# Performance work log

Measured on AMD Instinct MI355X. Metric: run time of the kernel, lower is better.

The kernel has to match this reference:

```python
import jax, jax.numpy as jnp
import numpy as np

INPUT_CHANNELS = 3

def setup_inputs() -> dict:
    key = jax.random.key(0)
    kx, ky = jax.random.split(key)
    x = jax.random.normal(kx, (8, 4096, 3), dtype=jnp.float32)
    y = jax.random.normal(ky, (8, 4096, 3), dtype=jnp.float32)
    return {"x": x, "y": y}

def reference(x, y):
    # Match torch: truncate both clouds to common num_points and input_channels.
    num_points = min(x.shape[1], y.shape[1])
    x = x[:, :num_points, :INPUT_CHANNELS]
    y = y[:, :num_points, :INPUT_CHANNELS]
    # pdist[b, i, j] = ||x_i||^2 + ||y_j||^2 - 2 x_i . y_j  (squared Euclidean)
    x2 = jnp.sum(x * x, axis=-1)          # [B, N]
    y2 = jnp.sum(y * y, axis=-1)          # [B, N]
    zz = jnp.einsum('bic,bjc->bij', x, y) # [B, N, N]
    pdist = x2[:, :, None] + y2[:, None, :] - 2.0 * zz
    # min over i (dim 1): nearest x for each y; min over j (dim 2): nearest y for each x
    loss = jnp.mean(jnp.min(pdist, axis=1)) + jnp.mean(jnp.min(pdist, axis=2))
    return loss * 0.005
```

## Files before the change

kernel.cpp:

```cpp
#include <hip/hip_runtime.h>

#define NPTS 4096
#define NB   8
#define TOT  (2 * NB * NPTS)

typedef __attribute__((ext_vector_type(8)))  short          bf16x8;
typedef __attribute__((ext_vector_type(8)))  unsigned short u16x8;
typedef __attribute__((ext_vector_type(16))) float          f32x16;

__device__ __forceinline__ unsigned short bf16_rne(float f) {
    unsigned u = __float_as_uint(f);
    u += 0x7FFFu + ((u >> 16) & 1u);
    return (unsigned short)(u >> 16);
}
__device__ __forceinline__ float bf16_f(unsigned short s) {
    return __uint_as_float(((unsigned)s) << 16);
}

__global__ __launch_bounds__(256) void prep_kernel(
    const float* __restrict__ x, const float* __restrict__ y,
    unsigned short* __restrict__ Aform, unsigned short* __restrict__ Bform,
    float* __restrict__ h32, unsigned* __restrict__ smax,
    float* __restrict__ out)
{
    int i   = blockIdx.x * 256 + threadIdx.x;
    int cid = i >> 12;
    int p   = i & 4095;
    const float* src = (cid < 8) ? x + ((size_t)cid * NPTS + p) * 3
                                 : y + ((size_t)(cid - 8) * NPTS + p) * 3;
    float c0 = src[0], c1 = src[1], c2 = src[2];
    float h  = -0.5f * (c0 * c0 + c1 * c1 + c2 * c2);

    unsigned short h0 = bf16_rne(c0), h1 = bf16_rne(c1), h2 = bf16_rne(c2);
    unsigned short l0 = bf16_rne(c0 - bf16_f(h0));
    unsigned short l1 = bf16_rne(c1 - bf16_f(h1));
    unsigned short l2 = bf16_rne(c2 - bf16_f(h2));
    unsigned short hh = bf16_rne(h);
    unsigned short hl = bf16_rne(h - bf16_f(hh));
    const unsigned short ONE = 0x3F80;

    u16x8 alo, ahi, blo, bhi;
    alo[0]=h0; alo[1]=h1; alo[2]=h2; alo[3]=l0; alo[4]=l1; alo[5]=l2; alo[6]=h0; alo[7]=h1;
    ahi[0]=h2; ahi[1]=ONE; ahi[2]=ONE; ahi[3]=0; ahi[4]=0; ahi[5]=0; ahi[6]=0; ahi[7]=0;
    blo[0]=h0; blo[1]=h1; blo[2]=h2; blo[3]=h0; blo[4]=h1; blo[5]=h2; blo[6]=l0; blo[7]=l1;
    bhi[0]=l2; bhi[1]=hh; bhi[2]=hl; bhi[3]=0; bhi[4]=0; bhi[5]=0; bhi[6]=0; bhi[7]=0;

    int u = p >> 5, pos = p & 31;
    size_t base = ((size_t)cid << 17) + (size_t)u * 1024 + (size_t)pos * 16;
    *(u16x8*)((char*)Aform + base)       = alo;
    *(u16x8*)((char*)Aform + base + 512) = ahi;
    *(u16x8*)((char*)Bform + base)       = blo;
    *(u16x8*)((char*)Bform + base + 512) = bhi;

    h32[i]  = h;
    smax[i] = 0u;
    if (i == 0) *out = 0.f;
}

__global__ __launch_bounds__(256, 2) void chamfer_mfma(
    const unsigned short* __restrict__ Aform,
    const unsigned short* __restrict__ Bform,
    unsigned* __restrict__ smax)
{
    __shared__ float buf[4][64][33];

    const int bid  = blockIdx.x;
    const int dirb = bid >> 6;
    const int sub  = bid & 63;
    const int iblk = sub >> 2;
    const int jq   = sub & 3;
    const int bcld = dirb ^ 8;

    const int tid = threadIdx.x;
    const int w   = tid >> 6;
    const int l   = tid & 63;
    const int g   = l >> 5;
    const int pos = l & 31;

    const char* Abase = (const char*)Aform + ((size_t)dirb << 17);
    const char* Bbase = (const char*)Bform + ((size_t)bcld << 17);

    const int it0 = iblk * 8 + w * 2;
    bf16x8 afr[2];
    #pragma unroll
    for (int t = 0; t < 2; ++t)
        afr[t] = *(const bf16x8*)(Abase + (size_t)(it0 + t) * 1024
                                        + (size_t)g * 512 + (size_t)pos * 16);

    f32x16 zc;
    #pragma unroll
    for (int r = 0; r < 16; ++r) zc[r] = 0.f;

    f32x16 run[2];
    #pragma unroll
    for (int t = 0; t < 2; ++t)
        #pragma unroll
        for (int r = 0; r < 16; ++r) run[t][r] = -3.0e38f;

    const char* Bq = Bbase + (size_t)(jq * 32) * 1024
                           + (size_t)g * 512 + (size_t)pos * 16;

    bf16x8 cb0 = *(const bf16x8*)(Bq);
    bf16x8 cb1 = *(const bf16x8*)(Bq + 1024);

    #pragma unroll 1
    for (int j = 0; j < 32; j += 2) {
        const int jn = (j + 2) & 31;
        bf16x8 nb0 = *(const bf16x8*)(Bq + (size_t)jn * 1024);
        bf16x8 nb1 = *(const bf16x8*)(Bq + (size_t)jn * 1024 + 1024);
        #pragma unroll
        for (int t = 0; t < 2; ++t) {
            f32x16 d0 = __builtin_amdgcn_mfma_f32_32x32x16_bf16(afr[t], cb0, zc, 0, 0, 0);
            f32x16 d1 = __builtin_amdgcn_mfma_f32_32x32x16_bf16(afr[t], cb1, zc, 0, 0, 0);
            #pragma unroll
            for (int r = 0; r < 16; ++r)
                run[t][r] = fmaxf(fmaxf(d0[r], d1[r]), run[t][r]);
        }
        cb0 = nb0; cb1 = nb1;
    }

    #pragma unroll
    for (int t = 0; t < 2; ++t)
        #pragma unroll
        for (int r = 0; r < 16; ++r) {
            int rowin = (r & 3) + 8 * (r >> 2) + 4 * g;
            buf[w][t * 32 + rowin][pos] = run[t][r];
        }
    __syncthreads();

    float m = buf[w][l][0];
    #pragma unroll
    for (int k = 1; k < 32; ++k) m = fmaxf(m, buf[w][l][k]);
    int idx = dirb * 4096 + iblk * 256 + w * 64 + l;
    unsigned bits = __float_as_uint(m);
    unsigned mu = (bits & 0x80000000u) ? ~bits : (bits | 0x80000000u);
    atomicMax(&smax[idx], mu);
}

__global__ __launch_bounds__(256) void reduce_kernel(
    const unsigned* __restrict__ smax,
    const float* __restrict__ h32,
    float* __restrict__ out)
{
    const int stride = 64 * 256;
    int tid = blockIdx.x * 256 + threadIdx.x;
    float s = 0.f;
    for (int k = tid; k < TOT; k += stride) {
        unsigned u = smax[k];
        unsigned bits = (u & 0x80000000u) ? (u & 0x7FFFFFFFu) : ~u;
        s += __uint_as_float(bits) + h32[k];
    }

    #pragma unroll
    for (int off = 32; off > 0; off >>= 1)
        s += __shfl_down(s, off);

    __shared__ float redb[4];
    const int lane = threadIdx.x & 63, wave = threadIdx.x >> 6;
    if (lane == 0) redb[wave] = s;
    __syncthreads();
    if (threadIdx.x == 0) {
        float t = redb[0] + redb[1] + redb[2] + redb[3];
        atomicAdd(out, t * (-2.0f * 0.005f / 32768.f));
    }
}

extern "C" void kernel_launch(void* const* d_in, const int* in_sizes, int n_in,
                              void* d_out, int out_size, void* d_ws, size_t ws_size,
                              hipStream_t stream) {
    const float* x = (const float*)d_in[0];
    const float* y = (const float*)d_in[1];
    float* out = (float*)d_out;

    unsigned short* Aform = (unsigned short*)d_ws;
    unsigned short* Bform = (unsigned short*)((char*)d_ws + (2u << 20));
    float*          h32   = (float*)((char*)d_ws + (4u << 20));
    unsigned*       smax  = (unsigned*)((char*)d_ws + (4u << 20) + (256u << 10));

    prep_kernel<<<dim3(TOT / 256), dim3(256), 0, stream>>>(x, y, Aform, Bform, h32, smax, out);
    chamfer_mfma<<<dim3(1024), dim3(256), 0, stream>>>(Aform, Bform, smax);
    reduce_kernel<<<dim3(64), dim3(256), 0, stream>>>(smax, h32, out);
}
```

Before: 74.45 us.

## Fuse A-fragment prep and final reduction into main MFMA kernel, drop split-j atomics

Each block now covers the full j range for 128 rows, so the cross-block atomicMax array and the separate reduce kernel go away. A fragments are built in-register straight from the raw inputs, and each block reduces its row mins and atomically adds one partial sum to the output. The B prefetch is made two iterations deep. Launches and workspace traffic drop, but the grid shrinks to 512 blocks of longer serial loops, which may hurt load balance and latency hiding.

```diff
diff --git a/kernel.cpp b/kernel.cpp
--- a/kernel.cpp
+++ b/kernel.cpp
@@ -2,11 +2,9 @@
 
 #define NPTS 4096
 #define NB   8
-#define TOT  (2 * NB * NPTS)
 
-typedef __attribute__((ext_vector_type(8)))  short          bf16x8;
-typedef __attribute__((ext_vector_type(8)))  unsigned short u16x8;
-typedef __attribute__((ext_vector_type(16))) float          f32x16;
+typedef __attribute__((ext_vector_type(8)))  short bf16x8;
+typedef __attribute__((ext_vector_type(16))) float f32x16;
 
 __device__ __forceinline__ unsigned short bf16_rne(float f) {
     unsigned u = __float_as_uint(f);
@@ -17,11 +15,10 @@
     return __uint_as_float(((unsigned)s) << 16);
 }
 
-__global__ __launch_bounds__(256) void prep_kernel(
+
+__global__ __launch_bounds__(256) void prep_b(
     const float* __restrict__ x, const float* __restrict__ y,
-    unsigned short* __restrict__ Aform, unsigned short* __restrict__ Bform,
-    float* __restrict__ h32, unsigned* __restrict__ smax,
-    float* __restrict__ out)
+    unsigned short* __restrict__ Bform)
 {
     int i   = blockIdx.x * 256 + threadIdx.x;
     int cid = i >> 12;
@@ -37,39 +34,29 @@
     unsigned short l2 = bf16_rne(c2 - bf16_f(h2));
     unsigned short hh = bf16_rne(h);
     unsigned short hl = bf16_rne(h - bf16_f(hh));
-    const unsigned short ONE = 0x3F80;
 
-    u16x8 alo, ahi, blo, bhi;
-    alo[0]=h0; alo[1]=h1; alo[2]=h2; alo[3]=l0; alo[4]=l1; alo[5]=l2; alo[6]=h0; alo[7]=h1;
-    ahi[0]=h2; ahi[1]=ONE; ahi[2]=ONE; ahi[3]=0; ahi[4]=0; ahi[5]=0; ahi[6]=0; ahi[7]=0;
-    blo[0]=h0; blo[1]=h1; blo[2]=h2; blo[3]=h0; blo[4]=h1; blo[5]=h2; blo[6]=l0; blo[7]=l1;
-    bhi[0]=l2; bhi[1]=hh; bhi[2]=hl; bhi[3]=0; bhi[4]=0; bhi[5]=0; bhi[6]=0; bhi[7]=0;
+    bf16x8 blo, bhi;
+    blo[0]=(short)h0; blo[1]=(short)h1; blo[2]=(short)h2; blo[3]=(short)h0;
+    blo[4]=(short)h1; blo[5]=(short)h2; blo[6]=(short)l0; blo[7]=(short)l1;
+    bhi[0]=(short)l2; bhi[1]=(short)hh; bhi[2]=(short)hl; bhi[3]=0;
+    bhi[4]=0; bhi[5]=0; bhi[6]=0; bhi[7]=0;
 
     int u = p >> 5, pos = p & 31;
     size_t base = ((size_t)cid << 17) + (size_t)u * 1024 + (size_t)pos * 16;
-    *(u16x8*)((char*)Aform + base)       = alo;
-    *(u16x8*)((char*)Aform + base + 512) = ahi;
-    *(u16x8*)((char*)Bform + base)       = blo;
-    *(u16x8*)((char*)Bform + base + 512) = bhi;
-
-    h32[i]  = h;
-    smax[i] = 0u;
-    if (i == 0) *out = 0.f;
+    *(bf16x8*)((char*)Bform + base)       = blo;
+    *(bf16x8*)((char*)Bform + base + 512) = bhi;
 }
 
-__global__ __launch_bounds__(256, 2) void chamfer_mfma(
-    const unsigned short* __restrict__ Aform,
+__global__ __launch_bounds__(256, 2) void chamfer_main(
+    const float* __restrict__ x, const float* __restrict__ y,
     const unsigned short* __restrict__ Bform,
-    unsigned* __restrict__ smax)
+    float* __restrict__ out)
 {
-    __shared__ float buf[4][64][33];
+    __shared__ float buf[4][32 * 33];
 
     const int bid  = blockIdx.x;
-    const int dirb = bid >> 6;
-    const int sub  = bid & 63;
-    const int iblk = sub >> 2;
-    const int jq   = sub & 3;
-    const int bcld = dirb ^ 8;
+    const int dirb = bid >> 5;
+    const int iblk = bid & 31;
 
     const int tid = threadIdx.x;
     const int w   = tid >> 6;
@@ -77,91 +64,75 @@
     const int g   = l >> 5;
     const int pos = l & 31;
 
-    const char* Abase = (const char*)Aform + ((size_t)dirb << 17);
-    const char* Bbase = (const char*)Bform + ((size_t)bcld << 17);
+    const float* Araw = (dirb < 8) ? x + (size_t)dirb * NPTS * 3
+                                   : y + (size_t)(dirb - 8) * NPTS * 3;
 
-    const int it0 = iblk * 8 + w * 2;
-    bf16x8 afr[2];
-    #pragma unroll
-    for (int t = 0; t < 2; ++t)
-        afr[t] = *(const bf16x8*)(Abase + (size_t)(it0 + t) * 1024
-                                        + (size_t)g * 512 + (size_t)pos * 16);
+    bf16x8 afr;
+    {
+        const float* ap = Araw + (size_t)(iblk * 128 + w * 32 + pos) * 3;
+        float c0 = ap[0], c1 = ap[1], c2 = ap[2];
+        unsigned short h0 = bf16_rne(c0), h1 = bf16_rne(c1), h2 = bf16_rne(c2);
+        unsigned short l0 = bf16_rne(c0 - bf16_f(h0));
+        unsigned short l1 = bf16_rne(c1 - bf16_f(h1));
+        unsigned short l2 = bf16_rne(c2 - bf16_f(h2));
+        const short ONE = (short)0x3F80;
+        bf16x8 alo, ahi;
+        alo[0]=(short)h0; alo[1]=(short)h1; alo[2]=(short)h2; alo[3]=(short)l0;
+        alo[4]=(short)l1; alo[5]=(short)l2; alo[6]=(short)h0; alo[7]=(short)h1;
+        ahi[0]=(short)h2; ahi[1]=ONE; ahi[2]=ONE; ahi[3]=0;
+        ahi[4]=0; ahi[5]=0; ahi[6]=0; ahi[7]=0;
+        #pragma unroll
+        for (int e = 0; e < 8; ++e) afr[e] = g ? ahi[e] : alo[e];
+    }
 
     f32x16 zc;
     #pragma unroll
     for (int r = 0; r < 16; ++r) zc[r] = 0.f;
 
-    f32x16 run[2];
+    f32x16 run;
     #pragma unroll
-    for (int t = 0; t < 2; ++t)
-        #pragma unroll
-        for (int r = 0; r < 16; ++r) run[t][r] = -3.0e38f;
+    for (int r = 0; r < 16; ++r) run[r] = -3.0e38f;
 
-    const char* Bq = Bbase + (size_t)(jq * 32) * 1024
-                           + (size_t)g * 512 + (size_t)pos * 16;
+    const char* Bbase = (const char*)Bform + ((size_t)(dirb ^ 8) << 17)
+                      + (size_t)g * 512 + (size_t)pos * 16;
 
-    bf16x8 cb0 = *(const bf16x8*)(Bq);
-    bf16x8 cb1 = *(const bf16x8*)(Bq + 1024);
+    bf16x8 cb0 = *(const bf16x8*)(Bbase);
+    bf16x8 cb1 = *(const bf16x8*)(Bbase + 1024);
+    bf16x8 pb0 = *(const bf16x8*)(Bbase + 2048);
+    bf16x8 pb1 = *(const bf16x8*)(Bbase + 3072);
 
     #pragma unroll 1
-    for (int j = 0; j < 32; j += 2) {
-        const int jn = (j + 2) & 31;
-        bf16x8 nb0 = *(const bf16x8*)(Bq + (size_t)jn * 1024);
-        bf16x8 nb1 = *(const bf16x8*)(Bq + (size_t)jn * 1024 + 1024);
+    for (int j = 0; j < 128; j += 2) {
+        int jn = j + 4; if (jn >= 128) jn -= 128;
+        bf16x8 nb0 = *(const bf16x8*)(Bbase + (size_t)jn * 1024);
+        bf16x8 nb1 = *(const bf16x8*)(Bbase + (size_t)jn * 1024 + 1024);
+        f32x16 d0 = __builtin_amdgcn_mfma_f32_32x32x16_bf16(afr, cb0, zc, 0, 0, 0);
+        f32x16 d1 = __builtin_amdgcn_mfma_f32_32x32x16_bf16(afr, cb1, zc, 0, 0, 0);
         #pragma unroll
-        for (int t = 0; t < 2; ++t) {
-            f32x16 d0 = __builtin_amdgcn_mfma_f32_32x32x16_bf16(afr[t], cb0, zc, 0, 0, 0);
-            f32x16 d1 = __builtin_amdgcn_mfma_f32_32x32x16_bf16(afr[t], cb1, zc, 0, 0, 0);
-            #pragma unroll
-            for (int r = 0; r < 16; ++r)
-                run[t][r] = fmaxf(fmaxf(d0[r], d1[r]), run[t][r]);
-        }
-        cb0 = nb0; cb1 = nb1;
+        for (int r = 0; r < 16; ++r)
+            run[r] = fmaxf(fmaxf(d0[r], d1[r]), run[r]);
+        cb0 = pb0; cb1 = pb1; pb0 = nb0; pb1 = nb1;
     }
 
     #pragma unroll
-    for (int t = 0; t < 2; ++t)
-        #pragma unroll
-        for (int r = 0; r < 16; ++r) {
-            int rowin = (r & 3) + 8 * (r >> 2) + 4 * g;
-            buf[w][t * 32 + rowin][pos] = run[t][r];
-        }
+    for (int r = 0; r < 16; ++r) {
+        int rowin = (r & 3) + 8 * (r >> 2) + 4 * g;
+        buf[w][rowin * 33 + pos] = run[r];
+    }
     __syncthreads();
 
-    float m = buf[w][l][0];
-    #pragma unroll
-    for (int k = 1; k < 32; ++k) m = fmaxf(m, buf[w][l][k]);
-    int idx = dirb * 4096 + iblk * 256 + w * 64 + l;
-    unsigned bits = __float_as_uint(m);
-    unsigned mu = (bits & 0x80000000u) ? ~bits : (bits | 0x80000000u);
-    atomicMax(&smax[idx], mu);
-}
-
-__global__ __launch_bounds__(256) void reduce_kernel(
-    const unsigned* __restrict__ smax,
-    const float* __restrict__ h32,
-    float* __restrict__ out)
-{
-    const int stride = 64 * 256;
-    int tid = blockIdx.x * 256 + threadIdx.x;
-    float s = 0.f;
-    for (int k = tid; k < TOT; k += stride) {
-        unsigned u = smax[k];
-        unsigned bits = (u & 0x80000000u) ? (u & 0x7FFFFFFFu) : ~u;
-        s += __uint_as_float(bits) + h32[k];
-    }
-
-    #pragma unroll
-    for (int off = 32; off > 0; off >>= 1)
-        s += __shfl_down(s, off);
-
-    __shared__ float redb[4];
-    const int lane = threadIdx.x & 63, wave = threadIdx.x >> 6;
-    if (lane == 0) redb[wave] = s;
-    __syncthreads();
-    if (threadIdx.x == 0) {
-        float t = redb[0] + redb[1] + redb[2] + redb[3];
-        atomicAdd(out, t * (-2.0f * 0.005f / 32768.f));
+    if (l < 32) {
+        float m = buf[w][l * 33];
+        #pragma unroll
+        for (int k = 1; k < 32; ++k) m = fmaxf(m, buf[w][l * 33 + k]);
+        const float* aq = Araw + (size_t)(iblk * 128 + w * 32 + l) * 3;
+        float a0 = aq[0], a1 = aq[1], a2 = aq[2];
+        float c  = m - 0.5f * (a0 * a0 + a1 * a1 + a2 * a2);
+        #pragma unroll
+        for (int mask = 16; mask >= 1; mask >>= 1)
+            c += __shfl_xor(c, mask);
+        if (l == 0)
+            atomicAdd(out, c * (-2.0f * 0.005f / 32768.f));
     }
 }
 
@@ -172,12 +143,9 @@
     const float* y = (const float*)d_in[1];
     float* out = (float*)d_out;
 
-    unsigned short* Aform = (unsigned short*)d_ws;
-    unsigned short* Bform = (unsigned short*)((char*)d_ws + (2u << 20));
-    float*          h32   = (float*)((char*)d_ws + (4u << 20));
-    unsigned*       smax  = (unsigned*)((char*)d_ws + (4u << 20) + (256u << 10));
+    unsigned short* Bform = (unsigned short*)d_ws;
 
-    prep_kernel<<<dim3(TOT / 256), dim3(256), 0, stream>>>(x, y, Aform, Bform, h32, smax, out);
-    chamfer_mfma<<<dim3(1024), dim3(256), 0, stream>>>(Aform, Bform, smax);
-    reduce_kernel<<<dim3(64), dim3(256), 0, stream>>>(smax, h32, out);
+    hipMemsetAsync(out, 0, sizeof(float), stream);
+    prep_b<<<dim3(256), dim3(256), 0, stream>>>(x, y, Bform);
+    chamfer_main<<<dim3(512), dim3(256), 0, stream>>>(x, y, Bform, out);
 }
```

Result: slower. 105.9 us (+42.3%).
